# Kernel optimization log

Measured on AMD Instinct MI355X. Metric: run time of the kernel, lower is better.

## Reference

```python
import jax, jax.numpy as jnp
import numpy as np

NUM_HEADS = 12
NUM_KV_HEADS = 2
HEAD_SIZE = 128
SCALE = 0.08838834764831845  # 1/sqrt(128)
GROUP = NUM_HEADS // NUM_KV_HEADS  # 6 query heads per kv head


def setup_inputs() -> dict:
    key = jax.random.key(0)
    kq, kk, kv = jax.random.split(key, 3)
    B, S = 1, 4096
    q = jax.random.normal(kq, (B, S, NUM_HEADS * HEAD_SIZE), dtype=jnp.float32)
    k = jax.random.normal(kk, (B, S, NUM_KV_HEADS * HEAD_SIZE), dtype=jnp.float32)
    v = jax.random.normal(kv, (B, S, NUM_KV_HEADS * HEAD_SIZE), dtype=jnp.float32)
    return {"q": q, "k": k, "v": v}


def reference(q, k, v):
    B, S, _ = q.shape
    qh = q.reshape(B, S, NUM_HEADS, HEAD_SIZE)            # [B,S,12,128]
    kh = k.reshape(B, S, NUM_KV_HEADS, HEAD_SIZE)         # [B,S,2,128]
    vh = v.reshape(B, S, NUM_KV_HEADS, HEAD_SIZE)
    # GQA: expand each kv head to its group of query heads
    kh = jnp.repeat(kh, GROUP, axis=2)                    # [B,S,12,128]
    vh = jnp.repeat(vh, GROUP, axis=2)
    scores = jnp.einsum("bqhd,bkhd->bhqk", qh, kh) * SCALE  # [B,12,S,S]
    causal = jnp.tril(jnp.ones((S, S), dtype=bool))
    scores = jnp.where(causal[None, None], scores, jnp.finfo(scores.dtype).min)
    probs = jax.nn.softmax(scores, axis=-1)
    out = jnp.einsum("bhqk,bkhd->bqhd", probs, vh)        # [B,S,12,128]
    return out.reshape(B, S, NUM_HEADS * HEAD_SIZE)
```

## Files before the change

### kernel.cpp

```cpp
#include <hip/hip_runtime.h>
#include <hip/hip_bf16.h>

typedef __attribute__((ext_vector_type(8)))  short  bf16x8;
typedef __attribute__((ext_vector_type(4)))  float  f32x4;
typedef __attribute__((ext_vector_type(16))) float  f32x16;
typedef __attribute__((ext_vector_type(4)))  int    i32x4;
typedef __attribute__((ext_vector_type(4)))  unsigned int u32x4;

#define NH   12
#define NKV  2
#define GRP  6
#define HD   128
#define SEQL 4096
#define QD   (NH*HD)
#define KD   (NKV*HD)
#define NT_KV (SEQL/32)
#define TILE_B 8192
#define WS_NEED ((size_t)2 * NKV * NT_KV * TILE_B)

static constexpr float SCL = 0.08838834764831845f * 1.44269504088896340736f;

static __device__ __forceinline__ unsigned int f2bf(float x) {
    union { __hip_bfloat16 h; unsigned short u; } cv;
    cv.h = __float2bfloat16(x);
    return (unsigned int)cv.u;
}
static __device__ __forceinline__ unsigned int pk2(float x, float y) {
    return f2bf(x) | (f2bf(y) << 16);
}

__global__ __launch_bounds__(256) void conv_k(const float* __restrict__ K,
                                              char* __restrict__ KW) {
    int id = blockIdx.x*256 + threadIdx.x;
    int l31  = id & 31;
    int hi   = (id >> 5) & 1;
    int c    = (id >> 6) & 7;
    int tile = (id >> 9) & 127;
    int kvh  = id >> 16;
    const float* src = K + (size_t)(tile*32 + l31)*KD + kvh*HD + c*16 + hi*8;
    const f32x4* s4 = reinterpret_cast<const f32x4*>(src);
    f32x4 a = s4[0], b = s4[1];
    bf16x8 t;
    t[0]=(short)f2bf(a[0]); t[1]=(short)f2bf(a[1]); t[2]=(short)f2bf(a[2]); t[3]=(short)f2bf(a[3]);
    t[4]=(short)f2bf(b[0]); t[5]=(short)f2bf(b[1]); t[6]=(short)f2bf(b[2]); t[7]=(short)f2bf(b[3]);
    *reinterpret_cast<bf16x8*>(KW + (size_t)(kvh*NT_KV + tile)*TILE_B
                               + c*1024 + (hi*32 + l31)*16) = t;
}

__global__ __launch_bounds__(256) void conv_v(const float* __restrict__ V,
                                              char* __restrict__ VW) {
    int id = blockIdx.x*256 + threadIdx.x;
    int d    = id & 127;
    int hi   = (id >> 7) & 1;
    int kc   = (id >> 8) & 1;
    int tile = (id >> 9) & 127;
    int kvh  = id >> 16;
    const float* vp = V + (size_t)(tile*32 + kc*16 + hi*8)*KD + kvh*HD + d;
    bf16x8 t;
    #pragma unroll
    for (int j = 0; j < 8; ++j) t[j] = (short)f2bf(vp[(size_t)j*KD]);
    char* dst = VW + (size_t)(kvh*NT_KV + tile)*TILE_B
              + (d>>5)*2048 + kc*1024 + (d&31)*32 + hi*16;
    *reinterpret_cast<bf16x8*>(dst) = t;
}

__global__ __launch_bounds__(128, 2) void gqa_attn_fwd(
        const float* __restrict__ Q,
        const char* __restrict__ KW,
        const char* __restrict__ VW,
        float* __restrict__ O)
{
    __shared__ float cO[32*128];
    __shared__ float cm[64];

    const int tid  = threadIdx.x;
    const int wv   = tid >> 6;
    const int lane = tid & 63;
    const int l31  = lane & 31;
    const int hi   = lane >> 5;

    const int bid = blockIdx.x;
    const int h   = bid % NH;
    const int qt  = (SEQL/32 - 1) - bid / NH;
    const int q0  = qt * 32;
    const int kvh = h / GRP;

    const char* kw0 = KW + (size_t)kvh*NT_KV*TILE_B;
    const char* vw0 = VW + (size_t)kvh*NT_KV*TILE_B;
    const int klocal = lane*16;
    const int vlocal = l31*32 + hi*16;

    bf16x8 qf[8];
    {
        const float* qp = Q + (size_t)(q0 + l31)*QD + h*HD + hi*8;
        #pragma unroll
        for (int c = 0; c < 8; ++c) {
            const f32x4* p4 = reinterpret_cast<const f32x4*>(qp + c*16);
            f32x4 a = p4[0], b = p4[1];
            bf16x8 f;
            f[0]=(short)f2bf(a[0]*SCL); f[1]=(short)f2bf(a[1]*SCL);
            f[2]=(short)f2bf(a[2]*SCL); f[3]=(short)f2bf(a[3]*SCL);
            f[4]=(short)f2bf(b[0]*SCL); f[5]=(short)f2bf(b[1]*SCL);
            f[6]=(short)f2bf(b[2]*SCL); f[7]=(short)f2bf(b[3]*SCL);
            qf[c] = f;
        }
    }

    f32x16 oa[4];
    #pragma unroll
    for (int dc = 0; dc < 4; ++dc)
        #pragma unroll
        for (int r = 0; r < 16; ++r) oa[dc][r] = 0.f;
    float m_run = -1e30f, lsum = 0.f;

    auto loadK = [&](int tt, bf16x8 (&kf)[8]) {
        const char* kt = kw0 + (size_t)tt*TILE_B + klocal;
        #pragma unroll
        for (int c = 0; c < 8; ++c)
            kf[c] = *reinterpret_cast<const bf16x8*>(kt + c*1024);
    };

    auto body = [&](int tcur, const bf16x8 (&kf)[8]) {
        const char* vt = vw0 + (size_t)tcur*TILE_B + vlocal;
        bf16x8 vf[8];
        #pragma unroll
        for (int i = 0; i < 8; ++i)
            vf[i] = *reinterpret_cast<const bf16x8*>(vt + (i>>1)*2048 + (i&1)*1024);

        f32x16 sA, sB;
        #pragma unroll
        for (int r = 0; r < 16; ++r) { sA[r] = 0.f; sB[r] = 0.f; }
        __builtin_amdgcn_s_setprio(1);
        #pragma unroll
        for (int c = 0; c < 4; ++c) {
            sA = __builtin_amdgcn_mfma_f32_32x32x16_bf16(kf[c],   qf[c],   sA, 0, 0, 0);
            sB = __builtin_amdgcn_mfma_f32_32x32x16_bf16(kf[c+4], qf[c+4], sB, 0, 0, 0);
        }
        __builtin_amdgcn_s_setprio(0);
        f32x16 s;
        #pragma unroll
        for (int r = 0; r < 16; ++r) s[r] = sA[r] + sB[r];

        if (tcur == qt) {
            const int qabs = q0 + l31;
            #pragma unroll
            for (int r = 0; r < 16; ++r) {
                const int kvi = q0 + (r&3) + 8*(r>>2) + 4*hi;
                if (kvi > qabs) s[r] = -1e30f;
            }
        }

        float m0 = fmaxf(s[0],s[1]),  m1 = fmaxf(s[2],s[3]);
        float m2 = fmaxf(s[4],s[5]),  m3 = fmaxf(s[6],s[7]);
        float m4 = fmaxf(s[8],s[9]),  m5 = fmaxf(s[10],s[11]);
        float m6 = fmaxf(s[12],s[13]), m7 = fmaxf(s[14],s[15]);
        m0 = fmaxf(m0,m1); m2 = fmaxf(m2,m3); m4 = fmaxf(m4,m5); m6 = fmaxf(m6,m7);
        float pmax = fmaxf(fmaxf(m0,m2), fmaxf(m4,m6));
        pmax = fmaxf(pmax, __shfl_xor(pmax, 32));

        if (__ballot(pmax > m_run + 8.0f)) {
            const float mnew  = fmaxf(m_run, pmax);
            const float alpha = exp2f(m_run - mnew);
            m_run = mnew;
            lsum *= alpha;
            #pragma unroll
            for (int r = 0; r < 16; ++r) {
                const float ar = __shfl(alpha, (r&3) + 8*(r>>2) + 4*hi, 64);
                #pragma unroll
                for (int dc = 0; dc < 4; ++dc) oa[dc][r] *= ar;
            }
        }

        float ps0 = 0.f, ps1 = 0.f;
        #pragma unroll
        for (int r = 0; r < 16; r += 2) {
            s[r]   = exp2f(s[r]   - m_run); ps0 += s[r];
            s[r+1] = exp2f(s[r+1] - m_run); ps1 += s[r+1];
        }
        lsum += ps0 + ps1;

        unsigned w0, w1, w2, w3, w4, w5, w6, w7;
        {
            unsigned a = pk2(s[0],  s[1]),  b = pk2(s[4],  s[5]);
            auto r0 = __builtin_amdgcn_permlane32_swap(a, b, false, false);
            w0 = r0[0]; w2 = r0[1];
            unsigned c2 = pk2(s[2],  s[3]),  d2 = pk2(s[6],  s[7]);
            auto r1 = __builtin_amdgcn_permlane32_swap(c2, d2, false, false);
            w1 = r1[0]; w3 = r1[1];
            unsigned e = pk2(s[8],  s[9]),  f = pk2(s[12], s[13]);
            auto r2 = __builtin_amdgcn_permlane32_swap(e, f, false, false);
            w4 = r2[0]; w6 = r2[1];
            unsigned g = pk2(s[10], s[11]), hh = pk2(s[14], s[15]);
            auto r3 = __builtin_amdgcn_permlane32_swap(g, hh, false, false);
            w5 = r3[0]; w7 = r3[1];
        }
        const bf16x8 pa0 = __builtin_bit_cast(bf16x8, (u32x4){w0, w1, w2, w3});
        const bf16x8 pa1 = __builtin_bit_cast(bf16x8, (u32x4){w4, w5, w6, w7});

        __builtin_amdgcn_s_setprio(1);
        #pragma unroll
        for (int dc = 0; dc < 4; ++dc) {
            oa[dc] = __builtin_amdgcn_mfma_f32_32x32x16_bf16(pa0, vf[dc*2],   oa[dc], 0, 0, 0);
            oa[dc] = __builtin_amdgcn_mfma_f32_32x32x16_bf16(pa1, vf[dc*2+1], oa[dc], 0, 0, 0);
        }
        __builtin_amdgcn_s_setprio(0);
    };

    bf16x8 kfA[8], kfB[8];
    int t = wv;
    if (t <= qt) loadK(t, kfA);
    while (t <= qt) {
        if (t + 2 <= qt) loadK(t + 2, kfB);
        body(t, kfA);
        t += 2;
        if (t > qt) break;
        if (t + 2 <= qt) loadK(t + 2, kfA);
        body(t, kfB);
        t += 2;
    }

    lsum += __shfl_xor(lsum, 32);

    if (wv == 1) {
        if (hi == 0) { cm[l31] = m_run; cm[32 + l31] = lsum; }
        #pragma unroll
        for (int r = 0; r < 16; ++r) {
            const int qr = (r&3) + 8*(r>>2) + 4*hi;
            #pragma unroll
            for (int dc = 0; dc < 4; ++dc)
                cO[qr*128 + dc*32 + l31] = oa[dc][r];
        }
    }
    __syncthreads();
    if (wv == 0) {
        const float m1 = cm[l31], l1 = cm[32 + l31];
        const float M  = fmaxf(m_run, m1);
        const float a0 = exp2f(m_run - M);
        const float a1 = exp2f(m1 - M);
        const float inv = 1.0f / (lsum*a0 + l1*a1);
        #pragma unroll
        for (int r = 0; r < 16; ++r) {
            const int qr = (r&3) + 8*(r>>2) + 4*hi;
            const float a0r = __shfl(a0, qr, 64);
            const float a1r = __shfl(a1, qr, 64);
            const float ivr = __shfl(inv, qr, 64);
            float* op = O + (size_t)(q0 + qr)*QD + h*HD + l31;
            #pragma unroll
            for (int dc = 0; dc < 4; ++dc) {
                const float merged = oa[dc][r]*a0r + cO[qr*128 + dc*32 + l31]*a1r;
                op[dc*32] = merged * ivr;
            }
        }
    }
}

__global__ __launch_bounds__(256) void gqa_attn_fwd_fb(
        const float* __restrict__ Q, const float* __restrict__ K,
        const float* __restrict__ V, float* __restrict__ O)
{
    __shared__ unsigned short K_lds[32*128];
    __shared__ unsigned short V_lds[32*128];

    const int tid  = threadIdx.x;
    const int wv   = tid >> 6;
    const int lane = tid & 63;
    const int lo   = lane & 15;
    const int g    = lane >> 4;

    const int bid = blockIdx.x;
    const int h   = bid % NH;
    const int qt  = (SEQL/64 - 1) - bid / NH;
    const int q0  = qt * 64;
    const int kvh = h / GRP;

    bf16x8 qf[4];
    {
        const int qrow = q0 + wv*16 + lo;
        const float* qp = Q + (size_t)qrow*QD + h*HD + g*8;
        #pragma unroll
        for (int c = 0; c < 4; ++c) {
            const f32x4* p = reinterpret_cast<const f32x4*>(qp + c*32);
            f32x4 a = p[0], b = p[1];
            bf16x8 f;
            f[0]=(short)f2bf(a[0]*SCL); f[1]=(short)f2bf(a[1]*SCL);
            f[2]=(short)f2bf(a[2]*SCL); f[3]=(short)f2bf(a[3]*SCL);
            f[4]=(short)f2bf(b[0]*SCL); f[5]=(short)f2bf(b[1]*SCL);
            f[6]=(short)f2bf(b[2]*SCL); f[7]=(short)f2bf(b[3]*SCL);
            qf[c] = f;
        }
    }

    f32x4 oa[8];
    #pragma unroll
    for (int i = 0; i < 8; ++i) oa[i] = (f32x4){0.f, 0.f, 0.f, 0.f};
    float m_run = -1e30f, lsum = 0.f;

    const int qmax_w = q0 + wv*16 + 15;
    const int nt = q0/32 + 2;

    for (int t = 0; t < nt; ++t) {
        const int kvb = t*32;
        __syncthreads();
        {
            const int row = tid >> 3;
            const int dc  = (tid & 7) * 16;
            const float* kp = K + (size_t)(kvb+row)*KD + kvh*HD + dc;
            const f32x4* kp4 = reinterpret_cast<const f32x4*>(kp);
            f32x4 a0 = kp4[0], a1 = kp4[1], a2 = kp4[2], a3 = kp4[3];
            bf16x8 t0, t1;
            t0[0]=(short)f2bf(a0[0]); t0[1]=(short)f2bf(a0[1]); t0[2]=(short)f2bf(a0[2]); t0[3]=(short)f2bf(a0[3]);
            t0[4]=(short)f2bf(a1[0]); t0[5]=(short)f2bf(a1[1]); t0[6]=(short)f2bf(a1[2]); t0[7]=(short)f2bf(a1[3]);
            t1[0]=(short)f2bf(a2[0]); t1[1]=(short)f2bf(a2[1]); t1[2]=(short)f2bf(a2[2]); t1[3]=(short)f2bf(a2[3]);
            t1[4]=(short)f2bf(a3[0]); t1[5]=(short)f2bf(a3[1]); t1[6]=(short)f2bf(a3[2]); t1[7]=(short)f2bf(a3[3]);
            char* kl = reinterpret_cast<char*>(K_lds);
            const int byte = row*256 + dc*2;
            const int swzw = (row & 7) << 4;
            *reinterpret_cast<bf16x8*>(kl + ((byte)      ^ swzw)) = t0;
            *reinterpret_cast<bf16x8*>(kl + ((byte + 16) ^ swzw)) = t1;
        }
        {
            const int kv0   = (tid >> 4) * 2;
            const int dbase = (tid & 15) * 8;
            const float* vp = V + (size_t)(kvb+kv0)*KD + kvh*HD + dbase;
            const f32x4* v0 = reinterpret_cast<const f32x4*>(vp);
            const f32x4* v1 = reinterpret_cast<const f32x4*>(vp + KD);
            f32x4 a0 = v0[0], a1 = v0[1], b0 = v1[0], b1 = v1[1];
            unsigned int* vf = reinterpret_cast<unsigned int*>(V_lds);
            #pragma unroll
            for (int i = 0; i < 8; ++i) {
                float x0 = (i < 4) ? a0[i] : a1[i-4];
                float x1 = (i < 4) ? b0[i] : b1[i-4];
                unsigned int pkv = f2bf(x0) | (f2bf(x1) << 16);
                const int d  = dbase + i;
                const int db = d >> 4, dl = d & 15;
                const int slot = (kv0 >> 3) ^ (d & 3) ^ (db & 3);
                const int byte = db*1024 + dl*64 + slot*16 + (kv0 & 7)*2;
                vf[byte >> 2] = pkv;
            }
        }
        __syncthreads();

        if (kvb > qmax_w) continue;

        f32x4 s0 = {0,0,0,0}, s1 = {0,0,0,0};
        {
            const char* kl = reinterpret_cast<const char*>(K_lds);
            const int r0 = lo, r1 = lo + 16;
            const int sw0 = (r0 & 7) << 4, sw1 = (r1 & 7) << 4;
            #pragma unroll
            for (int c = 0; c < 4; ++c) {
                bf16x8 ka = *reinterpret_cast<const bf16x8*>(kl + ((r0*256 + c*64 + g*16) ^ sw0));
                bf16x8 kb = *reinterpret_cast<const bf16x8*>(kl + ((r1*256 + c*64 + g*16) ^ sw1));
                s0 = __builtin_amdgcn_mfma_f32_16x16x32_bf16(ka, qf[c], s0, 0, 0, 0);
                s1 = __builtin_amdgcn_mfma_f32_16x16x32_bf16(kb, qf[c], s1, 0, 0, 0);
            }
        }

        const int qabs = q0 + wv*16 + lo;
        if (kvb + 31 > q0 + wv*16) {
            #pragma unroll
            for (int r = 0; r < 4; ++r) {
                if (kvb + 4*g + r      > qabs) s0[r] = -1e30f;
                if (kvb + 16 + 4*g + r > qabs) s1[r] = -1e30f;
            }
        }

        float pmax = fmaxf(fmaxf(fmaxf(s0[0],s0[1]), fmaxf(s0[2],s0[3])),
                           fmaxf(fmaxf(s1[0],s1[1]), fmaxf(s1[2],s1[3])));
        pmax = fmaxf(pmax, __shfl_xor(pmax, 16));
        pmax = fmaxf(pmax, __shfl_xor(pmax, 32));
        const float m_new = fmaxf(m_run, pmax);
        const float alpha = exp2f(m_run - m_new);
        float p0[4], p1[4];
        float psum = 0.f;
        #pragma unroll
        for (int r = 0; r < 4; ++r) {
            p0[r] = exp2f(s0[r] - m_new); psum += p0[r];
            p1[r] = exp2f(s1[r] - m_new); psum += p1[r];
        }
        psum += __shfl_xor(psum, 16);
        psum += __shfl_xor(psum, 32);
        lsum = lsum * alpha + psum;
        m_run = m_new;

        unsigned int pk0[2], pk1[2];
        pk0[0] = f2bf(p0[0]) | (f2bf(p0[1]) << 16);
        pk0[1] = f2bf(p0[2]) | (f2bf(p0[3]) << 16);
        pk1[0] = f2bf(p1[0]) | (f2bf(p1[1]) << 16);
        pk1[1] = f2bf(p1[2]) | (f2bf(p1[3]) << 16);

        i32x4 pav;
        #pragma unroll
        for (int pp = 0; pp < 4; ++pp) {
            const int src = lo + ((2*g + (pp >> 1)) & 3) * 16;
            const int v0s = __shfl((int)pk0[pp & 1], src, 64);
            const int v1s = __shfl((int)pk1[pp & 1], src, 64);
            pav[pp] = (g < 2) ? v0s : v1s;
        }
        const bf16x8 paf = __builtin_bit_cast(bf16x8, pav);

        float al[4];
        #pragma unroll
        for (int r = 0; r < 4; ++r) al[r] = __shfl(alpha, 4*g + r, 64);
        #pragma unroll
        for (int db = 0; db < 8; ++db) {
            oa[db][0] *= al[0]; oa[db][1] *= al[1];
            oa[db][2] *= al[2]; oa[db][3] *= al[3];
        }

        const char* vl = reinterpret_cast<const char*>(V_lds);
        #pragma unroll
        for (int db = 0; db < 8; ++db) {
            const int slot = g ^ (lo & 3) ^ (db & 3);
            bf16x8 vfr = *reinterpret_cast<const bf16x8*>(vl + db*1024 + lo*64 + slot*16);
            oa[db] = __builtin_amdgcn_mfma_f32_16x16x32_bf16(paf, vfr, oa[db], 0, 0, 0);
        }
    }

    float li[4];
    #pragma unroll
    for (int r = 0; r < 4; ++r) li[r] = 1.0f / __shfl(lsum, 4*g + r, 64);
    #pragma unroll
    for (int db = 0; db < 8; ++db) {
        #pragma unroll
        for (int r = 0; r < 4; ++r) {
            O[(size_t)(q0 + wv*16 + 4*g + r)*QD + h*HD + db*16 + lo] = oa[db][r] * li[r];
        }
    }
}

extern "C" void kernel_launch(void* const* d_in, const int* in_sizes, int n_in,
                              void* d_out, int out_size, void* d_ws, size_t ws_size,
                              hipStream_t stream) {
    const float* q = (const float*)d_in[0];
    const float* k = (const float*)d_in[1];
    const float* v = (const float*)d_in[2];
    float* out = (float*)d_out;
    (void)in_sizes; (void)n_in; (void)out_size;

    if (ws_size >= WS_NEED && d_ws != nullptr) {
        char* kw = (char*)d_ws;
        char* vw = kw + (size_t)NKV * NT_KV * TILE_B;
        conv_k<<<dim3(512), dim3(256), 0, stream>>>(k, kw);
        conv_v<<<dim3(512), dim3(256), 0, stream>>>(v, vw);
        gqa_attn_fwd<<<dim3((SEQL/32)*NH), dim3(128), 0, stream>>>(q, kw, vw, out);
    } else {
        gqa_attn_fwd_fb<<<dim3((SEQL/64)*NH), dim3(256), 0, stream>>>(q, k, v, out);
    }
}
```

Baseline: 105.0 us.

## Use hardware bf16 pack and exp2, remap blocks across XCDs, relax launch bounds

Replaces the software float-to-bf16 packing with the v_cvt_pk_bf16_f32 instruction and exp2f with the raw hardware exp2 builtin, which cuts VALU work in the softmax. Remaps block IDs so that each group of XCDs (assuming round-robin dispatch over 8 XCDs) serves a single KV head, aiming at better L2 reuse of K/V. It also drops the min-blocks-per-CU hint from launch bounds, which lets the compiler use more registers but may lower occupancy. The max reduction is rebalanced as well. The raw exp2 builtin skips denormal handling, which is acceptable here.

```diff
diff --git a/kernel.cpp b/kernel.cpp
--- a/kernel.cpp
+++ b/kernel.cpp
@@ -25,8 +25,10 @@
     cv.h = __float2bfloat16(x);
     return (unsigned int)cv.u;
 }
-static __device__ __forceinline__ unsigned int pk2(float x, float y) {
-    return f2bf(x) | (f2bf(y) << 16);
+static __device__ __forceinline__ unsigned int pkcvt(float lo, float hi) {
+    unsigned int r;
+    asm("v_cvt_pk_bf16_f32 %0, %1, %2" : "=v"(r) : "v"(lo), "v"(hi));
+    return r;
 }
 
 __global__ __launch_bounds__(256) void conv_k(const float* __restrict__ K,
@@ -64,7 +66,7 @@
     *reinterpret_cast<bf16x8*>(dst) = t;
 }
 
-__global__ __launch_bounds__(128, 2) void gqa_attn_fwd(
+__global__ __launch_bounds__(128) void gqa_attn_fwd(
         const float* __restrict__ Q,
         const char* __restrict__ KW,
         const char* __restrict__ VW,
@@ -80,10 +82,13 @@
     const int hi   = lane >> 5;
 
     const int bid = blockIdx.x;
-    const int h   = bid % NH;
-    const int qt  = (SEQL/32 - 1) - bid / NH;
+    const int xcd = bid & 7;
+    const int i8  = bid >> 3;
+    const int kvh = xcd >> 2;
+    const int j   = (xcd & 3)*192 + i8;
+    const int h   = kvh*GRP + (j % GRP);
+    const int qt  = (SEQL/32 - 1) - j / GRP;
     const int q0  = qt * 32;
-    const int kvh = h / GRP;
 
     const char* kw0 = KW + (size_t)kvh*NT_KV*TILE_B;
     const char* vw0 = VW + (size_t)kvh*NT_KV*TILE_B;
@@ -150,17 +155,16 @@
             }
         }
 
-        float m0 = fmaxf(s[0],s[1]),  m1 = fmaxf(s[2],s[3]);
-        float m2 = fmaxf(s[4],s[5]),  m3 = fmaxf(s[6],s[7]);
-        float m4 = fmaxf(s[8],s[9]),  m5 = fmaxf(s[10],s[11]);
-        float m6 = fmaxf(s[12],s[13]), m7 = fmaxf(s[14],s[15]);
-        m0 = fmaxf(m0,m1); m2 = fmaxf(m2,m3); m4 = fmaxf(m4,m5); m6 = fmaxf(m6,m7);
-        float pmax = fmaxf(fmaxf(m0,m2), fmaxf(m4,m6));
+        float m0 = fmaxf(fmaxf(s[0],s[1]),  fmaxf(s[2],s[3]));
+        float m1 = fmaxf(fmaxf(s[4],s[5]),  fmaxf(s[6],s[7]));
+        float m2 = fmaxf(fmaxf(s[8],s[9]),  fmaxf(s[10],s[11]));
+        float m3 = fmaxf(fmaxf(s[12],s[13]), fmaxf(s[14],s[15]));
+        float pmax = fmaxf(fmaxf(m0,m1), fmaxf(m2,m3));
         pmax = fmaxf(pmax, __shfl_xor(pmax, 32));
 
         if (__ballot(pmax > m_run + 8.0f)) {
             const float mnew  = fmaxf(m_run, pmax);
-            const float alpha = exp2f(m_run - mnew);
+            const float alpha = __builtin_amdgcn_exp2f(m_run - mnew);
             m_run = mnew;
             lsum *= alpha;
             #pragma unroll
@@ -174,23 +178,23 @@
         float ps0 = 0.f, ps1 = 0.f;
         #pragma unroll
         for (int r = 0; r < 16; r += 2) {
-            s[r]   = exp2f(s[r]   - m_run); ps0 += s[r];
-            s[r+1] = exp2f(s[r+1] - m_run); ps1 += s[r+1];
+            s[r]   = __builtin_amdgcn_exp2f(s[r]   - m_run); ps0 += s[r];
+            s[r+1] = __builtin_amdgcn_exp2f(s[r+1] - m_run); ps1 += s[r+1];
         }
         lsum += ps0 + ps1;
 
         unsigned w0, w1, w2, w3, w4, w5, w6, w7;
         {
-            unsigned a = pk2(s[0],  s[1]),  b = pk2(s[4],  s[5]);
+            unsigned a = pkcvt(s[0],  s[1]),  b = pkcvt(s[4],  s[5]);
             auto r0 = __builtin_amdgcn_permlane32_swap(a, b, false, false);
             w0 = r0[0]; w2 = r0[1];
-            unsigned c2 = pk2(s[2],  s[3]),  d2 = pk2(s[6],  s[7]);
+            unsigned c2 = pkcvt(s[2],  s[3]),  d2 = pkcvt(s[6],  s[7]);
             auto r1 = __builtin_amdgcn_permlane32_swap(c2, d2, false, false);
             w1 = r1[0]; w3 = r1[1];
-            unsigned e = pk2(s[8],  s[9]),  f = pk2(s[12], s[13]);
+            unsigned e = pkcvt(s[8],  s[9]),  f = pkcvt(s[12], s[13]);
             auto r2 = __builtin_amdgcn_permlane32_swap(e, f, false, false);
             w4 = r2[0]; w6 = r2[1];
-            unsigned g = pk2(s[10], s[11]), hh = pk2(s[14], s[15]);
+            unsigned g = pkcvt(s[10], s[11]), hh = pkcvt(s[14], s[15]);
             auto r3 = __builtin_amdgcn_permlane32_swap(g, hh, false, false);
             w5 = r3[0]; w7 = r3[1];
         }
@@ -235,8 +239,8 @@
     if (wv == 0) {
         const float m1 = cm[l31], l1 = cm[32 + l31];
         const float M  = fmaxf(m_run, m1);
-        const float a0 = exp2f(m_run - M);
-        const float a1 = exp2f(m1 - M);
+        const float a0 = __builtin_amdgcn_exp2f(m_run - M);
+        const float a1 = __builtin_amdgcn_exp2f(m1 - M);
         const float inv = 1.0f / (lsum*a0 + l1*a1);
         #pragma unroll
         for (int r = 0; r < 16; ++r) {
```

Result: slower. 171.5 us (+63.4%).
